# Optimization experiments

Hardware: AMD Instinct MI355X
Metric: run time of the kernel (lower is better)

## Reference

```python
import jax, jax.numpy as jnp
import numpy as np
import math

DIM = 512
HEADS = 8
DH = DIM // HEADS
B, C, H, W = 2, 512, 48, 48


def setup_inputs() -> dict:
    key = jax.random.key(0)
    k1, k2, k3, k4 = jax.random.split(key, 4)
    x = jax.random.normal(k1, (B, C, H, W), dtype=jnp.float32)
    # torch Linear weights: [out_features, in_features]
    w_qkv = jax.random.normal(k2, (3 * DIM, DIM), dtype=jnp.float32) * (DIM ** -0.5)
    w_out = jax.random.normal(k3, (DIM, DIM), dtype=jnp.float32) * (DIM ** -0.5)
    b_out = jax.random.normal(k4, (DIM,), dtype=jnp.float32) * 0.01
    wavelength = jnp.asarray(0.1, dtype=jnp.float32)
    return {"x": x, "w_qkv": w_qkv, "w_out": w_out, "b_out": b_out, "wavelength": wavelength}


def reference(x, w_qkv, w_out, b_out, wavelength):
    b, c, h, w = x.shape
    n = h * w
    scale = DH ** -0.5

    x_flat = x.reshape(b, c, n).transpose(0, 2, 1)  # [B, N, C]
    qkv = jnp.einsum('bnc,dc->bnd', x_flat, w_qkv)   # [B, N, 3*DIM]
    q, k, v = jnp.split(qkv, 3, axis=-1)

    def to_heads(t):
        return t.reshape(b, n, HEADS, DH).transpose(0, 2, 1, 3)  # [B, h, N, dh]

    q, k, v = to_heads(q), to_heads(k), to_heads(v)

    dots = jnp.einsum('bhid,bhjd->bhij', q, k) * scale  # [B, h, N, N]

    # Fresnel interference bias over spatial positions
    yy, xx = jnp.meshgrid(jnp.arange(h), jnp.arange(w), indexing='ij')
    positions = jnp.stack([yy, xx], axis=-1).astype(jnp.float32).reshape(-1, 2)  # [N, 2]
    pos_diff = positions[None, :, :] - positions[:, None, :]  # [N, N, 2]
    distances = jnp.sqrt(jnp.sum(pos_diff ** 2, axis=-1) + 1e-8)  # [N, N]
    phase = 2.0 * math.pi * distances / (jnp.abs(wavelength) * h + 1e-6)
    interference = jnp.cos(phase)

    dots = dots + interference[None, None, :, :] * 0.1
    attn = jax.nn.softmax(dots, axis=-1)
    out = jnp.einsum('bhij,bhjd->bhid', attn, v)  # [B, h, N, dh]
    out = out.transpose(0, 2, 1, 3).reshape(b, n, HEADS * DH)  # [B, N, DIM]
    out = jnp.einsum('bnd,od->bno', out, w_out) + b_out
    return out.transpose(0, 2, 1).reshape(b, c, h, w)
```

## Files before the change

### kernel.cpp

```cpp
#include <hip/hip_runtime.h>
#include <math.h>

#define BB 2
#define CC 512
#define NN 2304
#define NH 8
#define DD 512
#define D3 1536
#define WIDTH 48
#define C1 0.18033688f

#define KSPLIT 2
#define KTILES 18
#define NTBL 213

typedef _Float16 h8 __attribute__((ext_vector_type(8)));
typedef _Float16 h4 __attribute__((ext_vector_type(4)));
typedef _Float16 h2 __attribute__((ext_vector_type(2)));
typedef float f4 __attribute__((ext_vector_type(4)));

__device__ __forceinline__ void gload16(const void* g, void* s) {
  __builtin_amdgcn_global_load_lds(
      (const __attribute__((address_space(1))) unsigned int*)g,
      (__attribute__((address_space(3))) unsigned int*)s, 16, 0, 0);
}

__global__ __launch_bounds__(256) void prep_k(
    const float* __restrict__ x, const float* __restrict__ wq,
    const float* __restrict__ wo, const float* __restrict__ wavp,
    _Float16* __restrict__ xt, _Float16* __restrict__ wqh,
    _Float16* __restrict__ woh, _Float16* __restrict__ btf)
{
  __shared__ float Ls[32][33];
  const int t = threadIdx.x;
  const int e = blockIdx.x;

  if (e < 2304) {
    const int n0 = (e % 72) * 32;
    const int c0 = ((e / 72) % 16) * 32;
    const int b  = e / 1152;
#pragma unroll
    for (int p = 0; p < 4; ++p) {
      const int cl = (t >> 5) + p * 8, nl = t & 31;
      Ls[cl][nl] = x[((size_t)b * CC + c0 + cl) * NN + n0 + nl];
    }
    __syncthreads();
#pragma unroll
    for (int p = 0; p < 2; ++p) {
      const int nl = (t >> 4) + p * 16, cl = (t & 15) * 2;
      h2 v = {(_Float16)Ls[cl][nl], (_Float16)Ls[cl + 1][nl]};
      *(h2*)(xt + ((size_t)b * NN + n0 + nl) * CC + c0 + cl) = v;
    }
  } else if (e < 3328) {
    const int idx = (e - 2304) * 256 + t;
    const int NQ = (D3 * CC) / 4;
    if (idx < NQ) {
      float4 v = *(const float4*)(wq + (size_t)idx * 4);
      h4 o = {(_Float16)v.x, (_Float16)v.y, (_Float16)v.z, (_Float16)v.w};
      *(h4*)(wqh + (size_t)idx * 4) = o;
    } else {
      const int j = idx - NQ;
      float4 v = *(const float4*)(wo + (size_t)j * 4);
      h4 o = {(_Float16)v.x, (_Float16)v.y, (_Float16)v.z, (_Float16)v.w};
      *(h4*)(woh + (size_t)j * 4) = o;
    }
  } else {
    const int tbl = (e - 3328) * 2 + (t >> 7);
    if (tbl < NTBL) {
      const int tid = t & 127;
      const int dD = tbl / 3, qm = tbl % 3;
      const int qt0 = qm + 36;
      const int kt0 = qt0 - (dD - 35);
      const int w = tid >> 6, quad = (tid >> 4) & 3, l15 = tid & 15;
      const float pc = 6.283185307179586f / (fabsf(wavp[0]) * (float)WIDTH + 1e-6f);
      _Float16* o = btf + ((size_t)tbl * 128 + tid) * 32;
#pragma unroll
      for (int g = 0; g < 4; ++g) {
        h8 v;
#pragma unroll
        for (int el = 0; el < 8; ++el) {
          const int j = g * 8 + el;
          const int nt = j >> 4, mt = (j >> 2) & 3, r = j & 3;
          const int q = qt0 * 64 + w * 32 + nt * 16 + l15;
          const int k = kt0 * 64 + mt * 16 + quad * 4 + r;
          const float dy = (float)(q / WIDTH) - (float)(k / WIDTH);
          const float dx = (float)(q % WIDTH) - (float)(k % WIDTH);
          const float dist = sqrtf(dy * dy + dx * dx + 1e-8f);
          v[el] = (_Float16)(0.1f * __cosf(dist * pc) * 1.44269504f);
        }
        *(h8*)(o + g * 8) = v;
      }
    }
  }
}

__global__ __launch_bounds__(256) void qkv_gemm_k(
    const _Float16* __restrict__ xt, const _Float16* __restrict__ wqh,
    _Float16* __restrict__ qb, _Float16* __restrict__ kb,
    _Float16* __restrict__ vb)
{
  __shared__ _Float16 Xs[128][32];
  __shared__ _Float16 Ws[128][32];
  const int t = threadIdx.x;
  const int lane = t & 63, w = t >> 6;
  const int l15 = lane & 15, quad = lane >> 4;
  const int wm = w & 1, wn = w >> 1;
  const int n0 = blockIdx.x * 128;
  const int d0 = blockIdx.y * 128;
  const int b  = blockIdx.z;
  const bool isv = (d0 >= 2 * DD);
  const _Float16* xb = xt + (size_t)b * NN * CC;

  const int srow = lane >> 2, scol = (lane & 3) * 8;

  f4 acc[4][4];
#pragma unroll
  for (int mt = 0; mt < 4; ++mt)
#pragma unroll
    for (int nt = 0; nt < 4; ++nt) acc[mt][nt] = (f4)(0.f);

  for (int c0 = 0; c0 < CC; c0 += 32) {
#pragma unroll
    for (int r = 0; r < 2; ++r) {
      const int ci = w + r * 4;
      const int row = ci * 16 + srow;
      gload16(xb + (size_t)(n0 + row) * CC + c0 + scol, &Xs[0][0] + ci * 512);
      gload16(wqh + (size_t)(d0 + row) * CC + c0 + scol, &Ws[0][0] + ci * 512);
    }
    __syncthreads();

    h8 wfr[4], xfr[4];
#pragma unroll
    for (int mt = 0; mt < 4; ++mt)
      wfr[mt] = *(const h8*)&Ws[wm * 64 + mt * 16 + l15][quad * 8];
#pragma unroll
    for (int nt = 0; nt < 4; ++nt)
      xfr[nt] = *(const h8*)&Xs[wn * 64 + nt * 16 + l15][quad * 8];

    if (!isv) {
#pragma unroll
      for (int mt = 0; mt < 4; ++mt)
#pragma unroll
        for (int nt = 0; nt < 4; ++nt)
          acc[mt][nt] = __builtin_amdgcn_mfma_f32_16x16x32_f16(
              wfr[mt], xfr[nt], acc[mt][nt], 0, 0, 0);
    } else {
#pragma unroll
      for (int mt = 0; mt < 4; ++mt)
#pragma unroll
        for (int nt = 0; nt < 4; ++nt)
          acc[mt][nt] = __builtin_amdgcn_mfma_f32_16x16x32_f16(
              xfr[nt], wfr[mt], acc[mt][nt], 0, 0, 0);
    }
    __syncthreads();
  }

  if (!isv) {
    const int which = d0 >> 9;
    _Float16* buf = which == 0 ? qb : kb;
    const float qs = (which == 0) ? C1 : 1.0f;
    const int h = ((d0 & 511) >> 6) + wm;
#pragma unroll
    for (int mt = 0; mt < 4; ++mt) {
      const int dh = mt * 16 + quad * 4;
#pragma unroll
      for (int nt = 0; nt < 4; ++nt) {
        const int token = n0 + wn * 64 + nt * 16 + l15;
        h4 o = {(_Float16)(acc[mt][nt][0] * qs), (_Float16)(acc[mt][nt][1] * qs),
                (_Float16)(acc[mt][nt][2] * qs), (_Float16)(acc[mt][nt][3] * qs)};
        *(h4*)(buf + (((size_t)b * NH + h) * NN + token) * 64 + dh) = o;
      }
    }
  } else {
    const int h = ((d0 - 2 * DD) >> 6) + wm;
#pragma unroll
    for (int mt = 0; mt < 4; ++mt) {
      const int dh = mt * 16 + l15;
#pragma unroll
      for (int nt = 0; nt < 4; ++nt) {
        const int token = n0 + wn * 64 + nt * 16 + quad * 4;
        h4 o = {(_Float16)acc[mt][nt][0], (_Float16)acc[mt][nt][1],
                (_Float16)acc[mt][nt][2], (_Float16)acc[mt][nt][3]};
        *(h4*)(vb + (((size_t)b * NH + h) * 64 + dh) * NN + token) = o;
      }
    }
  }
}

__global__ __launch_bounds__(256, 3) void attn_k(
    const _Float16* __restrict__ qb, const _Float16* __restrict__ kb,
    const _Float16* __restrict__ vb, const _Float16* __restrict__ btf,
    _Float16* __restrict__ op, float* __restrict__ lp)
{
  __shared__ _Float16 Ks[64][72];
  __shared__ _Float16 Vs[64][72];
  __shared__ _Float16 Ps[128][72];

  const int t    = threadIdx.x;
  const int lane = t & 63;
  const int w    = t >> 6;
  const int l15  = lane & 15;
  const int quad = lane >> 4;
  const int qpair = blockIdx.x >> 1;
  const int kq    = blockIdx.x & 1;
  const int n0 = qpair * 128;
  const int qtile = qpair * 2 + (w >> 1);
  const int h  = blockIdx.y;
  const int b  = blockIdx.z;
  const size_t base = ((size_t)b * NH + h) * NN * 64;
  const _Float16* qp = qb + base;
  const _Float16* kp = kb + base;
  const _Float16* vp = vb + base;

  h8 qf[2][2];
#pragma unroll
  for (int nt = 0; nt < 2; ++nt)
#pragma unroll
    for (int ks = 0; ks < 2; ++ks)
      qf[nt][ks] = *(const h8*)(qp + (size_t)(n0 + w * 32 + nt * 16 + l15) * 64 +
                                ks * 32 + quad * 8);

  f4 oc[4][2];
#pragma unroll
  for (int mt = 0; mt < 4; ++mt)
#pragma unroll
    for (int nt = 0; nt < 2; ++nt) oc[mt][nt] = (f4)(0.f);
  float lac[2][2] = {};

  const int ktg0 = kq * KTILES;
  const _Float16* bp =
      btf + ((size_t)((qtile - ktg0 + 35) * 3 + qtile % 3) * 128 +
             (w & 1) * 64 + lane) * 32;

  h8 kr[2], vr[2], bfr[4];
  {
    const int k0 = ktg0 * 64;
#pragma unroll
    for (int r = 0; r < 2; ++r) {
      const int c = t + r * 256;
      const int row = c >> 3, off = (c & 7) * 8;
      kr[r] = *(const h8*)(kp + (size_t)(k0 + row) * 64 + off);
      vr[r] = *(const h8*)(vp + (size_t)row * NN + k0 + off);
    }
#pragma unroll
    for (int r = 0; r < 4; ++r) bfr[r] = *(const h8*)(bp + r * 8);
    bp -= 3 * 128 * 32;
  }

  for (int kt = 0; kt < KTILES; ++kt) {
    __syncthreads();
#pragma unroll
    for (int r = 0; r < 2; ++r) {
      const int c = t + r * 256;
      const int row = c >> 3, off = (c & 7) * 8;
      *(h8*)&Ks[row][off] = kr[r];
      *(h8*)&Vs[row][off] = vr[r];
    }
    __syncthreads();

    f4 st[4][2];
#pragma unroll
    for (int mt = 0; mt < 4; ++mt)
#pragma unroll
      for (int nt = 0; nt < 2; ++nt) {
        const int jb = nt * 16 + mt * 4;
        f4 s = {(float)bfr[jb >> 3][(jb & 7) + 0],
                (float)bfr[jb >> 3][(jb & 7) + 1],
                (float)bfr[jb >> 3][(jb & 7) + 2],
                (float)bfr[jb >> 3][(jb & 7) + 3]};
        st[mt][nt] = s;
      }

    if (kt + 1 < KTILES) {
      const int k0 = (ktg0 + kt + 1) * 64;
#pragma unroll
      for (int r = 0; r < 2; ++r) {
        const int c = t + r * 256;
        const int row = c >> 3, off = (c & 7) * 8;
        kr[r] = *(const h8*)(kp + (size_t)(k0 + row) * 64 + off);
        vr[r] = *(const h8*)(vp + (size_t)row * NN + k0 + off);
      }
#pragma unroll
      for (int r = 0; r < 4; ++r) bfr[r] = *(const h8*)(bp + r * 8);
      bp -= 3 * 128 * 32;
    }

#pragma unroll
    for (int ks = 0; ks < 2; ++ks) {
#pragma unroll
      for (int mt = 0; mt < 4; ++mt) {
        h8 kf = *(const h8*)&Ks[mt * 16 + l15][ks * 32 + quad * 8];
#pragma unroll
        for (int nt = 0; nt < 2; ++nt)
          st[mt][nt] = __builtin_amdgcn_mfma_f32_16x16x32_f16(
              kf, qf[nt][ks], st[mt][nt], 0, 0, 0);
      }
    }

#pragma unroll
    for (int nt = 0; nt < 2; ++nt) {
      const int q = w * 32 + nt * 16 + l15;
#pragma unroll
      for (int mt = 0; mt < 4; ++mt) {
        const float p0 = __builtin_exp2f(st[mt][nt][0]);
        const float p1 = __builtin_exp2f(st[mt][nt][1]);
        const float p2 = __builtin_exp2f(st[mt][nt][2]);
        const float p3 = __builtin_exp2f(st[mt][nt][3]);
        lac[nt][0] += p0 + p1;
        lac[nt][1] += p2 + p3;
        const auto plo = __builtin_amdgcn_cvt_pkrtz(p0, p1);
        const auto phi = __builtin_amdgcn_cvt_pkrtz(p2, p3);
        h4 pk = {(_Float16)plo[0], (_Float16)plo[1],
                 (_Float16)phi[0], (_Float16)phi[1]};
        *(h4*)&Ps[q][mt * 16 + quad * 4] = pk;
      }
    }

#pragma unroll
    for (int ks = 0; ks < 2; ++ks) {
      h8 pf[2];
#pragma unroll
      for (int nt = 0; nt < 2; ++nt)
        pf[nt] = *(const h8*)&Ps[w * 32 + nt * 16 + l15][ks * 32 + quad * 8];
#pragma unroll
      for (int mt = 0; mt < 4; ++mt) {
        h8 vf = *(const h8*)&Vs[mt * 16 + l15][ks * 32 + quad * 8];
#pragma unroll
        for (int nt = 0; nt < 2; ++nt)
          oc[mt][nt] = __builtin_amdgcn_mfma_f32_16x16x32_f16(
              vf, pf[nt], oc[mt][nt], 0, 0, 0);
      }
    }
  }

#pragma unroll
  for (int nt = 0; nt < 2; ++nt) {
    float l = lac[nt][0] + lac[nt][1];
    l += __shfl_xor(l, 16);
    l += __shfl_xor(l, 32);
    const float inv = 1.f / l;
    const int qi = n0 + w * 32 + nt * 16 + l15;
    _Float16* od = op + (size_t)kq * BB * NN * DD +
                   ((size_t)b * NN + qi) * DD + h * 64;
#pragma unroll
    for (int mt = 0; mt < 4; ++mt) {
      const int dh = mt * 16 + quad * 4;
      h4 o = {(_Float16)(oc[mt][nt][0] * inv), (_Float16)(oc[mt][nt][1] * inv),
              (_Float16)(oc[mt][nt][2] * inv), (_Float16)(oc[mt][nt][3] * inv)};
      *(h4*)(od + dh) = o;
    }
    if (quad == 0)
      lp[(size_t)kq * BB * NH * NN + ((size_t)b * NH + h) * NN + qi] = l;
  }
}

__global__ __launch_bounds__(256) void comb_k(
    const _Float16* __restrict__ op, const float* __restrict__ lp,
    _Float16* __restrict__ ho)
{
  const int idx = blockIdx.x * 256 + threadIdx.x;
  const int d8 = idx & 63;
  const int bn = idx >> 6;
  const int n = bn % NN, b = bn / NN;
  const int h = d8 >> 3;
  const size_t SL = (size_t)BB * NH * NN;
  const size_t SO = (size_t)BB * NN * DD;
  const size_t li = ((size_t)b * NH + h) * NN + n;
  const float l0 = lp[li];
  const float l1 = lp[SL + li];
  const float inv = 1.f / (l0 + l1);
  const float w0 = l0 * inv, w1 = l1 * inv;
  h8 o0 = *(const h8*)(op + (size_t)bn * DD + d8 * 8);
  h8 o1 = *(const h8*)(op + SO + (size_t)bn * DD + d8 * 8);
  h8 r;
#pragma unroll
  for (int i = 0; i < 8; ++i)
    r[i] = (_Float16)((float)o0[i] * w0 + (float)o1[i] * w1);
  *(h8*)(ho + (size_t)bn * DD + d8 * 8) = r;
}

__global__ __launch_bounds__(64) void out_gemm_k(
    const _Float16* __restrict__ ho, const _Float16* __restrict__ woh,
    const float* __restrict__ bias, float* __restrict__ out)
{
  __shared__ _Float16 Hs[64][32];
  __shared__ _Float16 Ws2[64][32];
  const int t = threadIdx.x;
  const int l15 = t & 15, quad = t >> 4;
  const int n0 = blockIdx.x * 64;
  const int o0 = blockIdx.y * 64;
  const int b  = blockIdx.z;
  const int srow = t >> 2, scol = (t & 3) * 8;

  f4 acc[4][4];
#pragma unroll
  for (int mt = 0; mt < 4; ++mt)
#pragma unroll
    for (int nt = 0; nt < 4; ++nt) acc[mt][nt] = (f4)(0.f);

  for (int c0 = 0; c0 < DD; c0 += 32) {
#pragma unroll
    for (int ci = 0; ci < 4; ++ci) {
      const int row = ci * 16 + srow;
      gload16(ho + ((size_t)b * NN + n0 + row) * DD + c0 + scol,
              &Hs[0][0] + ci * 512);
      gload16(woh + (size_t)(o0 + row) * DD + c0 + scol,
              &Ws2[0][0] + ci * 512);
    }
    __syncthreads();
    h8 hf[4], wf[4];
#pragma unroll
    for (int mt = 0; mt < 4; ++mt)
      hf[mt] = *(const h8*)&Hs[mt * 16 + l15][quad * 8];
#pragma unroll
    for (int nt = 0; nt < 4; ++nt)
      wf[nt] = *(const h8*)&Ws2[nt * 16 + l15][quad * 8];
#pragma unroll
    for (int mt = 0; mt < 4; ++mt)
#pragma unroll
      for (int nt = 0; nt < 4; ++nt)
        acc[mt][nt] = __builtin_amdgcn_mfma_f32_16x16x32_f16(
            hf[mt], wf[nt], acc[mt][nt], 0, 0, 0);
    __syncthreads();
  }

#pragma unroll
  for (int nt = 0; nt < 4; ++nt) {
    const int o = o0 + nt * 16 + l15;
    const float bv = bias[o];
#pragma unroll
    for (int mt = 0; mt < 4; ++mt) {
      const int token = n0 + mt * 16 + quad * 4;
      float4 v = {acc[mt][nt][0] + bv, acc[mt][nt][1] + bv,
                  acc[mt][nt][2] + bv, acc[mt][nt][3] + bv};
      *(float4*)(out + ((size_t)b * DD + o) * NN + token) = v;
    }
  }
}

extern "C" void kernel_launch(void* const* d_in, const int* in_sizes, int n_in,
                              void* d_out, int out_size, void* d_ws, size_t ws_size,
                              hipStream_t stream)
{
  (void)in_sizes; (void)n_in; (void)out_size; (void)ws_size;
  const float* x     = (const float*)d_in[0];
  const float* w_qkv = (const float*)d_in[1];
  const float* w_out = (const float*)d_in[2];
  const float* b_out = (const float*)d_in[3];
  const float* wav   = (const float*)d_in[4];
  float* out = (float*)d_out;

  const size_t SZ  = (size_t)BB * NH * NN * 64;
  const size_t BTF = (size_t)NTBL * 128 * 32;

  _Float16* qb  = (_Float16*)d_ws;
  _Float16* kb  = qb + SZ;
  _Float16* vb  = kb + SZ;
  _Float16* btf = vb + SZ;
  _Float16* op  = btf + BTF;
  float*    lpf = (float*)(op + 2 * SZ);
  _Float16* woh = (_Float16*)(lpf + 2 * (size_t)BB * NH * NN);
  _Float16* ho  = qb;
  _Float16* xt  = op;
  _Float16* wqh = op + SZ;

  prep_k    <<<dim3(2304 + 1024 + 107), 256, 0, stream>>>(x, w_qkv, w_out, wav,
                                                          xt, wqh, woh, btf);
  qkv_gemm_k<<<dim3(NN / 128, D3 / 128, BB), 256, 0, stream>>>(xt, wqh, qb, kb, vb);
  attn_k    <<<dim3((NN / 128) * KSPLIT, NH, BB), 256, 0, stream>>>(qb, kb, vb, btf, op, lpf);
  comb_k    <<<dim3((BB * NN * 64) / 256), 256, 0, stream>>>(op, lpf, ho);
  out_gemm_k<<<dim3(NN / 64, DD / 64, BB), 64, 0, stream>>>(ho, woh, b_out, out);
}
```

Before: 162.6 us.

## Double-buffer K/V tiles via direct global-to-LDS loads; enlarge output GEMM blocks

Measured after the change: 165.2 us. About the same (+1.6%).

```diff
diff --git a/kernel.cpp b/kernel.cpp
--- a/kernel.cpp
+++ b/kernel.cpp
@@ -192,8 +192,8 @@
     const _Float16* __restrict__ vb, const _Float16* __restrict__ btf,
     _Float16* __restrict__ op, float* __restrict__ lp)
 {
-  __shared__ _Float16 Ks[64][72];
-  __shared__ _Float16 Vs[64][72];
+  __shared__ _Float16 Kb[2][8][64][8];
+  __shared__ _Float16 Vb[2][8][64][8];
   __shared__ _Float16 Ps[128][72];
 
   const int t    = threadIdx.x;
@@ -232,31 +232,33 @@
       btf + ((size_t)((qtile - ktg0 + 35) * 3 + qtile % 3) * 128 +
              (w & 1) * 64 + lane) * 32;
 
-  h8 kr[2], vr[2], bfr[4];
+  h8 bfr[4];
   {
     const int k0 = ktg0 * 64;
 #pragma unroll
     for (int r = 0; r < 2; ++r) {
-      const int c = t + r * 256;
-      const int row = c >> 3, off = (c & 7) * 8;
-      kr[r] = *(const h8*)(kp + (size_t)(k0 + row) * 64 + off);
-      vr[r] = *(const h8*)(vp + (size_t)row * NN + k0 + off);
+      const int ch = w + r * 4;
+      gload16(kp + (size_t)(k0 + lane) * 64 + ch * 8, &Kb[0][ch][0][0]);
+      gload16(vp + (size_t)lane * NN + k0 + ch * 8, &Vb[0][ch][0][0]);
     }
 #pragma unroll
     for (int r = 0; r < 4; ++r) bfr[r] = *(const h8*)(bp + r * 8);
     bp -= 3 * 128 * 32;
   }
+  __syncthreads();
 
   for (int kt = 0; kt < KTILES; ++kt) {
-    __syncthreads();
-#pragma unroll
-    for (int r = 0; r < 2; ++r) {
-      const int c = t + r * 256;
-      const int row = c >> 3, off = (c & 7) * 8;
-      *(h8*)&Ks[row][off] = kr[r];
-      *(h8*)&Vs[row][off] = vr[r];
-    }
-    __syncthreads();
+    const int cur = kt & 1;
+
+    if (kt + 1 < KTILES) {
+      const int k0 = (ktg0 + kt + 1) * 64;
+#pragma unroll
+      for (int r = 0; r < 2; ++r) {
+        const int ch = w + r * 4;
+        gload16(kp + (size_t)(k0 + lane) * 64 + ch * 8, &Kb[cur ^ 1][ch][0][0]);
+        gload16(vp + (size_t)lane * NN + k0 + ch * 8, &Vb[cur ^ 1][ch][0][0]);
+      }
+    }
 
     f4 st[4][2];
 #pragma unroll
@@ -270,16 +272,7 @@
                 (float)bfr[jb >> 3][(jb & 7) + 3]};
         st[mt][nt] = s;
       }
-
     if (kt + 1 < KTILES) {
-      const int k0 = (ktg0 + kt + 1) * 64;
-#pragma unroll
-      for (int r = 0; r < 2; ++r) {
-        const int c = t + r * 256;
-        const int row = c >> 3, off = (c & 7) * 8;
-        kr[r] = *(const h8*)(kp + (size_t)(k0 + row) * 64 + off);
-        vr[r] = *(const h8*)(vp + (size_t)row * NN + k0 + off);
-      }
 #pragma unroll
       for (int r = 0; r < 4; ++r) bfr[r] = *(const h8*)(bp + r * 8);
       bp -= 3 * 128 * 32;
@@ -289,7 +282,7 @@
     for (int ks = 0; ks < 2; ++ks) {
 #pragma unroll
       for (int mt = 0; mt < 4; ++mt) {
-        h8 kf = *(const h8*)&Ks[mt * 16 + l15][ks * 32 + quad * 8];
+        h8 kf = *(const h8*)&Kb[cur][ks * 4 + quad][mt * 16 + l15][0];
 #pragma unroll
         for (int nt = 0; nt < 2; ++nt)
           st[mt][nt] = __builtin_amdgcn_mfma_f32_16x16x32_f16(
@@ -324,13 +317,15 @@
         pf[nt] = *(const h8*)&Ps[w * 32 + nt * 16 + l15][ks * 32 + quad * 8];
 #pragma unroll
       for (int mt = 0; mt < 4; ++mt) {
-        h8 vf = *(const h8*)&Vs[mt * 16 + l15][ks * 32 + quad * 8];
+        h8 vf = *(const h8*)&Vb[cur][ks * 4 + quad][mt * 16 + l15][0];
 #pragma unroll
         for (int nt = 0; nt < 2; ++nt)
           oc[mt][nt] = __builtin_amdgcn_mfma_f32_16x16x32_f16(
               vf, pf[nt], oc[mt][nt], 0, 0, 0);
       }
     }
+
+    __syncthreads();
   }
 
 #pragma unroll
@@ -379,58 +374,61 @@
   *(h8*)(ho + (size_t)bn * DD + d8 * 8) = r;
 }
 
-__global__ __launch_bounds__(64) void out_gemm_k(
+__global__ __launch_bounds__(256) void out_gemm_k(
     const _Float16* __restrict__ ho, const _Float16* __restrict__ woh,
     const float* __restrict__ bias, float* __restrict__ out)
 {
-  __shared__ _Float16 Hs[64][32];
+  __shared__ _Float16 Hs[128][32];
   __shared__ _Float16 Ws2[64][32];
   const int t = threadIdx.x;
-  const int l15 = t & 15, quad = t >> 4;
-  const int n0 = blockIdx.x * 64;
+  const int lane = t & 63, w = t >> 6;
+  const int l15 = lane & 15, quad = lane >> 4;
+  const int wm = w & 1, wn = w >> 1;
+  const int n0 = blockIdx.x * 128;
   const int o0 = blockIdx.y * 64;
   const int b  = blockIdx.z;
-  const int srow = t >> 2, scol = (t & 3) * 8;
-
-  f4 acc[4][4];
+  const int srow = lane >> 2, scol = (lane & 3) * 8;
+
+  f4 acc[4][2];
 #pragma unroll
   for (int mt = 0; mt < 4; ++mt)
 #pragma unroll
-    for (int nt = 0; nt < 4; ++nt) acc[mt][nt] = (f4)(0.f);
+    for (int nt = 0; nt < 2; ++nt) acc[mt][nt] = (f4)(0.f);
 
   for (int c0 = 0; c0 < DD; c0 += 32) {
 #pragma unroll
-    for (int ci = 0; ci < 4; ++ci) {
+    for (int r = 0; r < 2; ++r) {
+      const int ci = w + r * 4;
       const int row = ci * 16 + srow;
       gload16(ho + ((size_t)b * NN + n0 + row) * DD + c0 + scol,
               &Hs[0][0] + ci * 512);
-      gload16(woh + (size_t)(o0 + row) * DD + c0 + scol,
-              &Ws2[0][0] + ci * 512);
-    }
-    __syncthreads();
-    h8 hf[4], wf[4];
+    }
+    gload16(woh + (size_t)(o0 + w * 16 + srow) * DD + c0 + scol,
+            &Ws2[0][0] + w * 512);
+    __syncthreads();
+    h8 hf[4], wf[2];
 #pragma unroll
     for (int mt = 0; mt < 4; ++mt)
-      hf[mt] = *(const h8*)&Hs[mt * 16 + l15][quad * 8];
-#pragma unroll
-    for (int nt = 0; nt < 4; ++nt)
-      wf[nt] = *(const h8*)&Ws2[nt * 16 + l15][quad * 8];
+      hf[mt] = *(const h8*)&Hs[wm * 64 + mt * 16 + l15][quad * 8];
+#pragma unroll
+    for (int nt = 0; nt < 2; ++nt)
+      wf[nt] = *(const h8*)&Ws2[wn * 32 + nt * 16 + l15][quad * 8];
 #pragma unroll
     for (int mt = 0; mt < 4; ++mt)
 #pragma unroll
-      for (int nt = 0; nt < 4; ++nt)
+      for (int nt = 0; nt < 2; ++nt)
         acc[mt][nt] = __builtin_amdgcn_mfma_f32_16x16x32_f16(
             hf[mt], wf[nt], acc[mt][nt], 0, 0, 0);
     __syncthreads();
   }
 
 #pragma unroll
-  for (int nt = 0; nt < 4; ++nt) {
-    const int o = o0 + nt * 16 + l15;
+  for (int nt = 0; nt < 2; ++nt) {
+    const int o = o0 + wn * 32 + nt * 16 + l15;
     const float bv = bias[o];
 #pragma unroll
     for (int mt = 0; mt < 4; ++mt) {
-      const int token = n0 + mt * 16 + quad * 4;
+      const int token = n0 + wm * 64 + mt * 16 + quad * 4;
       float4 v = {acc[mt][nt][0] + bv, acc[mt][nt][1] + bv,
                   acc[mt][nt][2] + bv, acc[mt][nt][3] + bv};
       *(float4*)(out + ((size_t)b * DD + o) * NN + token) = v;
@@ -469,5 +467,5 @@
   qkv_gemm_k<<<dim3(NN / 128, D3 / 128, BB), 256, 0, stream>>>(xt, wqh, qb, kb, vb);
   attn_k    <<<dim3((NN / 128) * KSPLIT, NH, BB), 256, 0, stream>>>(qb, kb, vb, btf, op, lpf);
   comb_k    <<<dim3((BB * NN * 64) / 256), 256, 0, stream>>>(op, lpf, ho);
-  out_gemm_k<<<dim3(NN / 64, DD / 64, BB), 64, 0, stream>>>(ho, woh, b_out, out);
-}
+  out_gemm_k<<<dim3(NN / 128, DD / 64, BB), 256, 0, stream>>>(ho, woh, b_out, out);
+}
```
